# Kernel tuning notes

Hardware: AMD Instinct MI355X
Metric: run time of the kernel (lower is better)

## Reference

```python
import jax, jax.numpy as jnp
import numpy as np

GROUPS = 32
N_HEADS = 16
EPS = 1e-5


def setup_inputs() -> dict:
    key = jax.random.key(0)
    ks = jax.random.split(key, 5)
    b, c, t = 4, 1024, 1024
    return {
        "x": jax.random.normal(ks[0], (b, c, t), dtype=jnp.float32),
        "gn_weight": jnp.ones((c,), dtype=jnp.float32),
        "gn_bias": jnp.zeros((c,), dtype=jnp.float32),
        "qkv_w": jax.random.normal(ks[1], (3 * c, c), dtype=jnp.float32) * (c ** -0.5),
        "qkv_b": jax.random.normal(ks[2], (3 * c,), dtype=jnp.float32) * 0.02,
        "proj_w": jax.random.normal(ks[3], (c, c), dtype=jnp.float32) * (c ** -0.5),
        "proj_b": jax.random.normal(ks[4], (c,), dtype=jnp.float32) * 0.02,
    }


def _group_norm(x, weight, bias):
    # x: [b, c, t]; GroupNorm32 computes stats in float32 (already fp32 here)
    b, c, t = x.shape
    xg = x.reshape(b, GROUPS, c // GROUPS, t)
    mean = xg.mean(axis=(2, 3), keepdims=True)
    var = xg.var(axis=(2, 3), keepdims=True)
    xn = ((xg - mean) * jax.lax.rsqrt(var + EPS)).reshape(b, c, t)
    return xn * weight[None, :, None] + bias[None, :, None]


def reference(x, gn_weight, gn_bias, qkv_w, qkv_b, proj_w, proj_b):
    b, c, t = x.shape
    xn = _group_norm(x, gn_weight, gn_bias)
    # 1x1 Conv1d == channel matmul: [3c, c] x [b, c, t] -> [b, 3c, t]
    qkv = jnp.einsum('oc,bct->bot', qkv_w, xn) + qkv_b[None, :, None]
    ch = c // N_HEADS
    # legacy per-head interleaved layout: reshape to [b*H, 3*ch, t], split
    qkv = qkv.reshape(b * N_HEADS, 3 * ch, t)
    q, k, v = qkv[:, :ch], qkv[:, ch:2 * ch], qkv[:, 2 * ch:]
    scale = ch ** -0.25  # 1/sqrt(sqrt(ch)), applied to both q and k
    weight = jnp.einsum('bct,bcs->bts', q * scale, k * scale)  # [b*H, t, t]
    weight = jax.nn.softmax(weight.astype(jnp.float32), axis=-1).astype(weight.dtype)
    a = jnp.einsum('bts,bcs->bct', weight, v).reshape(b, c, t)
    h = jnp.einsum('oc,bct->bot', proj_w, a) + proj_b[None, :, None]
    return x + h
```

## Files before the change

### kernel.cpp

```cpp
#include <hip/hip_runtime.h>
#include <hip/hip_bf16.h>

typedef __bf16 bf16;
typedef __bf16 bf16x2 __attribute__((ext_vector_type(2)));
typedef __bf16 bf16x4 __attribute__((ext_vector_type(4)));
typedef __bf16 bf16x8 __attribute__((ext_vector_type(8)));
typedef float  f32x4  __attribute__((ext_vector_type(4)));

static __device__ __forceinline__ f32x4 mfma16(bf16x8 a, bf16x8 b, f32x4 c) {
  return __builtin_amdgcn_mfma_f32_16x16x32_bf16(a, b, c, 0, 0, 0);
}

static __device__ __forceinline__ void gload_lds16(const bf16* g, bf16* l) {
  __builtin_amdgcn_global_load_lds(
      (const __attribute__((address_space(1))) void*)g,
      (__attribute__((address_space(3))) void*)l, 16, 0, 0);
}

#define VMCNT0() asm volatile("s_waitcnt vmcnt(0)" ::: "memory")
#define BARRIER()                                        \
  do {                                                   \
    asm volatile("" ::: "memory");                       \
    __builtin_amdgcn_s_barrier();                        \
    asm volatile("" ::: "memory");                       \
  } while (0)

__global__ __launch_bounds__(256) void cvt2_kernel(const float* __restrict__ wa,
                                                   bf16* __restrict__ oa,
                                                   const float* __restrict__ wb,
                                                   bf16* __restrict__ ob) {
  int i = blockIdx.x * 256 + threadIdx.x;
  const int na4 = 3072 * 1024 / 4;
  const float* src; bf16* dst;
  if (i < na4) { src = wa; dst = oa; }
  else         { src = wb; dst = ob; i -= na4; }
  float4 v = ((const float4*)src)[i];
  bf16x4 o = { (bf16)v.x, (bf16)v.y, (bf16)v.z, (bf16)v.w };
  *(bf16x4*)(dst + 4ll * i) = o;
}

__global__ __launch_bounds__(512) void gn_kernel(const float* __restrict__ x,
                                                 const float* __restrict__ w,
                                                 const float* __restrict__ bias,
                                                 bf16* __restrict__ xnT) {
  int id = blockIdx.x;
  int b = id >> 7, g = (id >> 2) & 31, qtr = id & 3;
  const float* xb = x + ((size_t)b * 1024 + g * 32) * 1024;
  int tid = threadIdx.x;
  float s = 0.f, sq = 0.f;
  const float4* x4 = (const float4*)xb;
  for (int i = tid; i < 8192; i += 512) {
    float4 v = x4[i];
    s  += v.x + v.y + v.z + v.w;
    sq += v.x * v.x + v.y * v.y + v.z * v.z + v.w * v.w;
  }
#pragma unroll
  for (int off = 32; off; off >>= 1) { s += __shfl_down(s, off); sq += __shfl_down(sq, off); }
  __shared__ float red[16];
  int wv = tid >> 6;
  if ((tid & 63) == 0) { red[wv] = s; red[8 + wv] = sq; }
  __syncthreads();
  s = 0.f; sq = 0.f;
#pragma unroll
  for (int i = 0; i < 8; ++i) { s += red[i]; sq += red[8 + i]; }
  float mean = s * (1.f / 32768.f);
  float var  = sq * (1.f / 32768.f) - mean * mean;
  float rstd = rsqrtf(var + 1e-5f);

  __shared__ bf16 tile[64][36];
  int c = tid >> 4, q = tid & 15;
  int r = tid >> 3, q2 = tid & 7;
  float wc = w[g * 32 + c] * rstd;
  float fb = bias[g * 32 + c] - mean * wc;
  for (int t0 = qtr * 256; t0 < qtr * 256 + 256; t0 += 64) {
    float4 v = *(const float4*)(xb + (size_t)c * 1024 + t0 + q * 4);
    tile[q * 4 + 0][c] = (bf16)(v.x * wc + fb);
    tile[q * 4 + 1][c] = (bf16)(v.y * wc + fb);
    tile[q * 4 + 2][c] = (bf16)(v.z * wc + fb);
    tile[q * 4 + 3][c] = (bf16)(v.w * wc + fb);
    __syncthreads();
    *(bf16x4*)&xnT[((size_t)b * 1024 + t0 + r) * 1024 + g * 32 + q2 * 4] =
        *(bf16x4*)&tile[r][q2 * 4];
    __syncthreads();
  }
}

__global__ __launch_bounds__(512, 1) void qkv_kernel(
    const bf16* __restrict__ A, const bf16* __restrict__ Bw,
    const float* __restrict__ bias,
    bf16* __restrict__ qkT, bf16* __restrict__ vC) {
  extern __shared__ __align__(16) bf16 smem[];

  int tid = threadIdx.x, wid = tid >> 6, lane = tid & 63;
  int l15 = lane & 15, l4 = lane >> 4;
  int wr = wid >> 2, wc = wid & 3;
  int rsw = (l15 & 7) << 4;

  int sid = (blockIdx.x & 7) * 32 + (blockIdx.x >> 3);
  int bx = sid & 15, by = (sid >> 4) & 3, z = sid >> 6;
  int m0 = by * 256, n0 = bx * 192;
  const bf16* Ab = A + (size_t)z * 1024 * 1024 + (size_t)m0 * 1024;
  const bf16* Bb = Bw + (size_t)n0 * 1024;

  int srow = tid >> 3;
  int csw  = (tid & 7) ^ (srow & 7);
  auto stageA = [&](int d, int h, int kt) {
    bf16* dst = smem + d * 16384 + h * 8192;
    const bf16* src = Ab + (size_t)(h * 128) * 1024 + kt * 64 + csw * 8;
#pragma unroll
    for (int L = 0; L < 2; ++L)
      gload_lds16(src + (size_t)(L * 64 + srow) * 1024, dst + (L * 512 + wid * 64) * 8);
  };
  auto stageB = [&](int d, int kt) {
    bf16* dst = smem + 32768 + d * 12288;
    const bf16* src = Bb + kt * 64 + csw * 8;
#pragma unroll
    for (int L = 0; L < 3; ++L)
      gload_lds16(src + (size_t)(L * 64 + srow) * 1024, dst + (L * 512 + wid * 64) * 8);
  };

  f32x4 acc[8][3] = {};

  stageA(0, 0, 0); stageA(0, 1, 0); stageB(0, 0);
  VMCNT0();
  BARRIER();

  for (int t = 0; t < 16; ++t) {
    int d = t & 1;
    const char* Ab8 = (const char*)smem + d * 32768 + wr * 16384;
    const char* Bb8 = (const char*)smem + 65536 + d * 24576;

    bf16x8 bfr[3][2], af[4][2];
#pragma unroll
    for (int ni = 0; ni < 3; ++ni) {
      int rb = (wc * 48 + ni * 16 + l15) * 128;
#pragma unroll
      for (int kk = 0; kk < 2; ++kk)
        bfr[ni][kk] = *(const bf16x8*)(Bb8 + rb + ((kk * 64 + l4 * 16) ^ rsw));
    }
#pragma unroll
    for (int mi = 0; mi < 4; ++mi) {
      int rb = (mi * 16 + l15) * 128;
#pragma unroll
      for (int kk = 0; kk < 2; ++kk)
        af[mi][kk] = *(const bf16x8*)(Ab8 + rb + ((kk * 64 + l4 * 16) ^ rsw));
    }
    if (t < 15) { stageA(d ^ 1, 0, t + 1); stageA(d ^ 1, 1, t + 1); }
#pragma unroll
    for (int mi = 0; mi < 4; ++mi)
#pragma unroll
      for (int ni = 0; ni < 3; ++ni)
#pragma unroll
        for (int kk = 0; kk < 2; ++kk)
          acc[mi][ni] = mfma16(af[mi][kk], bfr[ni][kk], acc[mi][ni]);

#pragma unroll
    for (int mi = 0; mi < 4; ++mi) {
      int rb = ((4 + mi) * 16 + l15) * 128;
#pragma unroll
      for (int kk = 0; kk < 2; ++kk)
        af[mi][kk] = *(const bf16x8*)(Ab8 + rb + ((kk * 64 + l4 * 16) ^ rsw));
    }
    if (t < 15) stageB(d ^ 1, t + 1);
#pragma unroll
    for (int mi = 0; mi < 4; ++mi)
#pragma unroll
      for (int ni = 0; ni < 3; ++ni)
#pragma unroll
        for (int kk = 0; kk < 2; ++kk)
          acc[4 + mi][ni] = mfma16(af[mi][kk], bfr[ni][kk], acc[4 + mi][ni]);

    VMCNT0();
    BARRIER();
  }

  const float scale = 0.35355339059327373f;
  int h = bx;
#pragma unroll
  for (int ni = 0; ni < 3; ++ni) {
    int oin = wc * 48 + ni * 16;
    float bv = bias[n0 + oin + l15];
#pragma unroll
    for (int mi = 0; mi < 8; ++mi) {
      int tb = m0 + wr * 128 + mi * 16 + l4 * 4;
      f32x4 v = acc[mi][ni];
      if (oin < 128) {
#pragma unroll
        for (int i = 0; i < 4; ++i)
          qkT[((size_t)z * 1024 + tb + i) * 2048 + h * 128 + oin + l15] =
              (bf16)((v[i] + bv) * scale);
      } else {
        bf16x4 st = { (bf16)(v[0] + bv), (bf16)(v[1] + bv),
                      (bf16)(v[2] + bv), (bf16)(v[3] + bv) };
        *(bf16x4*)&vC[(((size_t)z * 16 + h) * 64 + (oin - 128 + l15)) * 1024 + tb] = st;
      }
    }
  }
}

template <int MODE>
__global__ __launch_bounds__(256) void gemm_kernel(
    const bf16* __restrict__ A, const bf16* __restrict__ Bw,
    const float* __restrict__ bias,
    bf16* __restrict__ qkT, bf16* __restrict__ vC,
    const float* __restrict__ xres, float* __restrict__ out) {
  __shared__ bf16 At[128 * 32];
  __shared__ bf16 Bt[128 * 32];
  int tid = threadIdx.x;
  int wid = tid >> 6, lane = tid & 63;
  int l15 = lane & 15, l4 = lane >> 4;
  int wm = wid >> 1, wn = wid & 1;
  int z = blockIdx.z;
  int m0 = blockIdx.y * 128, n0 = blockIdx.x * 128;
  const bf16* Ab = A + (size_t)z * 1024 * 1024 + (size_t)m0 * 1024;
  const bf16* Bb = Bw + (size_t)n0 * 1024;

  f32x4 acc[4][4] = {};

  for (int k0 = 0; k0 < 1024; k0 += 32) {
#pragma unroll
    for (int j = 0; j < 2; ++j) {
      int slot = j * 256 + tid;
      int row  = slot >> 2;
      int ck   = (slot & 3) ^ ((row >> 1) & 3);
      gload_lds16(Ab + (size_t)row * 1024 + k0 + ck * 8, At + (size_t)(j * 256 + wid * 64) * 8);
      gload_lds16(Bb + (size_t)row * 1024 + k0 + ck * 8, Bt + (size_t)(j * 256 + wid * 64) * 8);
    }
    __syncthreads();
    bf16x8 af[4], bfr[4];
#pragma unroll
    for (int mi = 0; mi < 4; ++mi) {
      int row = wm * 64 + mi * 16 + l15;
      int ck  = l4 ^ ((row >> 1) & 3);
      af[mi] = *(const bf16x8*)(At + row * 32 + ck * 8);
    }
#pragma unroll
    for (int nf = 0; nf < 4; ++nf) {
      int row = wn * 64 + nf * 16 + l15;
      int ck  = l4 ^ ((row >> 1) & 3);
      bfr[nf] = *(const bf16x8*)(Bt + row * 32 + ck * 8);
    }
#pragma unroll
    for (int mi = 0; mi < 4; ++mi)
#pragma unroll
      for (int nf = 0; nf < 4; ++nf)
        acc[mi][nf] = mfma16(af[mi], bfr[nf], acc[mi][nf]);
    __syncthreads();
  }

  if (MODE == 1) {
#pragma unroll
    for (int nf = 0; nf < 4; ++nf) {
      int o = n0 + wn * 64 + nf * 16 + l15;
      float bv = bias[o];
#pragma unroll
      for (int mi = 0; mi < 4; ++mi) {
        int tb = m0 + wm * 64 + mi * 16 + l4 * 4;
        size_t base = ((size_t)z * 1024 + o) * 1024 + tb;
        float4 xr = *(const float4*)(xres + base);
        f32x4 v = acc[mi][nf];
        float4 ov = { xr.x + v[0] + bv, xr.y + v[1] + bv,
                      xr.z + v[2] + bv, xr.w + v[3] + bv };
        *(float4*)(out + base) = ov;
      }
    }
  }
}

__global__ __launch_bounds__(512, 4) void attn_kernel(const bf16* __restrict__ qkT,
                                                      const bf16* __restrict__ vC,
                                                      bf16* __restrict__ aT) {
  __shared__ __align__(16) bf16 Kt[2][64 * 64];
  __shared__ __align__(16) bf16 Vt[2][64 * 64];
  __shared__ __align__(16) bf16 Pt[8][16 * 64];

  int id = blockIdx.x;
  int sid = (id & 7) * 64 + (id >> 3);
  int head = sid >> 3, tblk = sid & 7;
  int b = head >> 4, h = head & 15;
  int t0 = tblk * 128;
  int tid = threadIdx.x, wid = tid >> 6, lane = tid & 63;
  int l15 = lane & 15, l4 = lane >> 4;
  int trow = t0 + wid * 16;

  const bf16* kbase = qkT + (size_t)b * 1024 * 2048 + h * 128 + 64;
  const bf16* vbase = vC + (size_t)(b * 16 + h) * 64 * 1024;
  char* Pw = (char*)Pt[wid];
  int rsw = (l15 & 7) << 4;
  char* PwRow = Pw + l15 * 128;

  const bf16* qrow = qkT + ((size_t)b * 1024 + trow + l15) * 2048 + h * 128;
  bf16x8 qf[2];
#pragma unroll
  for (int kb = 0; kb < 2; ++kb) qf[kb] = *(const bf16x8*)(qrow + kb * 32 + l4 * 8);

  int rl = lane >> 3;
  int scol = (((lane & 7) * 16) ^ (rl << 4)) >> 1;
  int r8 = wid * 8 + rl;
  auto stage = [&](int buf, int st) {
    int s0 = st * 64;
    gload_lds16(kbase + (size_t)(s0 + r8) * 2048 + scol, &Kt[buf][wid * 512]);
    gload_lds16(vbase + (size_t)r8 * 1024 + s0 + scol, &Vt[buf][wid * 512]);
  };

  float m_run = -1e30f, l_run = 0.f;
  f32x4 oacc[4] = {};

  stage(0, 0);
  __syncthreads();

  for (int st = 0; st < 16; ++st) {
    int cur = st & 1;
    if (st < 15) stage(cur ^ 1, st + 1);

    const char* Kb = (const char*)Kt[cur];
    f32x4 sf[4];
#pragma unroll
    for (int nf = 0; nf < 4; ++nf) sf[nf] = (f32x4){0.f, 0.f, 0.f, 0.f};
    __builtin_amdgcn_s_setprio(1);
#pragma unroll
    for (int nf = 0; nf < 4; ++nf) {
      int rr = nf * 16 + l15;
#pragma unroll
      for (int kb = 0; kb < 2; ++kb) {
        bf16x8 kf = *(const bf16x8*)(Kb + rr * 128 + ((kb * 64 + l4 * 16) ^ rsw));
        sf[nf] = mfma16(kf, qf[kb], sf[nf]);
      }
    }
    __builtin_amdgcn_s_setprio(0);

    float mb;
    {
      float a0 = fmaxf(fmaxf(sf[0][0], sf[0][1]), fmaxf(sf[0][2], sf[0][3]));
      float a1 = fmaxf(fmaxf(sf[1][0], sf[1][1]), fmaxf(sf[1][2], sf[1][3]));
      float a2 = fmaxf(fmaxf(sf[2][0], sf[2][1]), fmaxf(sf[2][2], sf[2][3]));
      float a3 = fmaxf(fmaxf(sf[3][0], sf[3][1]), fmaxf(sf[3][2], sf[3][3]));
      mb = fmaxf(fmaxf(a0, a1), fmaxf(a2, a3));
    }
    mb = fmaxf(mb, __shfl_xor(mb, 16));
    mb = fmaxf(mb, __shfl_xor(mb, 32));
    if (!__all(mb - m_run <= 8.f)) {
      float mn = fmaxf(m_run, mb);
      float corr = __expf(m_run - mn);
      m_run = mn;
      l_run *= corr;
#pragma unroll
      for (int cf = 0; cf < 4; ++cf)
#pragma unroll
        for (int i = 0; i < 4; ++i) oacc[cf][i] *= corr;
    }
    float sb = 0.f;
#pragma unroll
    for (int nf = 0; nf < 4; ++nf) {
      float p0 = __expf(sf[nf][0] - m_run), p1 = __expf(sf[nf][1] - m_run);
      float p2 = __expf(sf[nf][2] - m_run), p3 = __expf(sf[nf][3] - m_run);
      sb += (p0 + p1) + (p2 + p3);
      int off = nf * 32 + l4 * 8;
      *(bf16x4*)(PwRow + (off ^ rsw)) = (bf16x4){ (bf16)p0, (bf16)p1, (bf16)p2, (bf16)p3 };
    }
    sb += __shfl_xor(sb, 16);
    sb += __shfl_xor(sb, 32);
    l_run += sb;

    const char* Vb = (const char*)Vt[cur];
    __builtin_amdgcn_s_setprio(1);
#pragma unroll
    for (int kb = 0; kb < 2; ++kb) {
      bf16x8 pf = *(const bf16x8*)(Pw + l15 * 128 + ((kb * 64 + l4 * 16) ^ rsw));
#pragma unroll
      for (int cf = 0; cf < 4; ++cf) {
        int rr = cf * 16 + l15;
        bf16x8 vf = *(const bf16x8*)(Vb + rr * 128 + ((kb * 64 + l4 * 16) ^ rsw));
        oacc[cf] = mfma16(vf, pf, oacc[cf]);
      }
    }
    __builtin_amdgcn_s_setprio(0);
    __syncthreads();
  }

  float rdiv = 1.f / l_run;
  int t = trow + l15;
#pragma unroll
  for (int cf = 0; cf < 4; ++cf) {
    bf16x4 ov = { (bf16)(oacc[cf][0] * rdiv), (bf16)(oacc[cf][1] * rdiv),
                  (bf16)(oacc[cf][2] * rdiv), (bf16)(oacc[cf][3] * rdiv) };
    *(bf16x4*)&aT[((size_t)b * 1024 + t) * 1024 + h * 64 + cf * 16 + l4 * 4] = ov;
  }
}

extern "C" void kernel_launch(void* const* d_in, const int* in_sizes, int n_in,
                              void* d_out, int out_size, void* d_ws, size_t ws_size,
                              hipStream_t stream) {
  const float* x      = (const float*)d_in[0];
  const float* gw     = (const float*)d_in[1];
  const float* gb     = (const float*)d_in[2];
  const float* qkv_w  = (const float*)d_in[3];
  const float* qkv_b  = (const float*)d_in[4];
  const float* proj_w = (const float*)d_in[5];
  const float* proj_b = (const float*)d_in[6];
  float* out = (float*)d_out;

  char* ws = (char*)d_ws;
  bf16* wq_bf = (bf16*)(ws);
  bf16* wp_bf = (bf16*)(ws + 6ll  * 1024 * 1024);
  bf16* xnT   = (bf16*)(ws + 8ll  * 1024 * 1024);
  bf16* qkT   = (bf16*)(ws + 16ll * 1024 * 1024);
  bf16* vC    = (bf16*)(ws + 32ll * 1024 * 1024);
  bf16* aT    = (bf16*)(ws + 40ll * 1024 * 1024);

  hipFuncSetAttribute(reinterpret_cast<const void*>(qkv_kernel),
                      hipFuncAttributeMaxDynamicSharedMemorySize, 114688);

  cvt2_kernel<<<dim3(4096), dim3(256), 0, stream>>>(qkv_w, wq_bf, proj_w, wp_bf);
  gn_kernel<<<dim3(512), dim3(512), 0, stream>>>(x, gw, gb, xnT);
  qkv_kernel<<<dim3(256), dim3(512), 114688, stream>>>(xnT, wq_bf, qkv_b, qkT, vC);
  attn_kernel<<<dim3(512), dim3(512), 0, stream>>>(qkT, vC, aT);
  gemm_kernel<1><<<dim3(8, 8, 4), dim3(256), 0, stream>>>(aT, wp_bf, proj_b, nullptr, nullptr, x, out);
}
```

Baseline: 108.4 us.

## Triple-buffer A tiles in QKV GEMM with partial vmcnt waits

Restructures the QKV GEMM main loop so A tiles are triple-buffered and B tiles double-buffered. Loads are issued two k-steps ahead for A, and the wait becomes vmcnt(4) instead of a full drain, so global-to-LDS loads overlap more of the MFMA work. LDS use grows from 112 KB to 144 KB per block. This is still within the 160 KB LDS per CU but leaves less headroom, and correctness depends on the vmcnt accounting matching the load issue order.

```diff
diff --git a/kernel.cpp b/kernel.cpp
--- a/kernel.cpp
+++ b/kernel.cpp
@@ -18,6 +18,7 @@
 }
 
 #define VMCNT0() asm volatile("s_waitcnt vmcnt(0)" ::: "memory")
+#define VMCNT4() asm volatile("s_waitcnt vmcnt(4)" ::: "memory")
 #define BARRIER()                                        \
   do {                                                   \
     asm volatile("" ::: "memory");                       \
@@ -104,15 +105,18 @@
 
   int srow = tid >> 3;
   int csw  = (tid & 7) ^ (srow & 7);
-  auto stageA = [&](int d, int h, int kt) {
-    bf16* dst = smem + d * 16384 + h * 8192;
-    const bf16* src = Ab + (size_t)(h * 128) * 1024 + kt * 64 + csw * 8;
-#pragma unroll
-    for (int L = 0; L < 2; ++L)
-      gload_lds16(src + (size_t)(L * 64 + srow) * 1024, dst + (L * 512 + wid * 64) * 8);
+  auto stageA = [&](int d, int kt) {
+    bf16* dst = smem + d * 16384;
+    const bf16* src = Ab + kt * 64 + csw * 8;
+#pragma unroll
+    for (int hh = 0; hh < 2; ++hh)
+#pragma unroll
+      for (int L = 0; L < 2; ++L)
+        gload_lds16(src + (size_t)(hh * 128 + L * 64 + srow) * 1024,
+                    dst + hh * 8192 + (L * 512 + wid * 64) * 8);
   };
   auto stageB = [&](int d, int kt) {
-    bf16* dst = smem + 32768 + d * 12288;
+    bf16* dst = smem + 49152 + d * 12288;
     const bf16* src = Bb + kt * 64 + csw * 8;
 #pragma unroll
     for (int L = 0; L < 3; ++L)
@@ -121,58 +125,63 @@
 
   f32x4 acc[8][3] = {};
 
-  stageA(0, 0, 0); stageA(0, 1, 0); stageB(0, 0);
+  auto compute = [&](int ta, int tb) {
+    const char* Ab8 = (const char*)smem + ta * 32768 + wr * 16384;
+    const char* Bb8 = (const char*)smem + 98304 + tb * 24576;
+    bf16x8 bfr[3][2], af[4][2];
+#pragma unroll
+    for (int ni = 0; ni < 3; ++ni) {
+      int rb = (wc * 48 + ni * 16 + l15) * 128;
+#pragma unroll
+      for (int kk = 0; kk < 2; ++kk)
+        bfr[ni][kk] = *(const bf16x8*)(Bb8 + rb + ((kk * 64 + l4 * 16) ^ rsw));
+    }
+#pragma unroll
+    for (int mi = 0; mi < 4; ++mi) {
+      int rb = (mi * 16 + l15) * 128;
+#pragma unroll
+      for (int kk = 0; kk < 2; ++kk)
+        af[mi][kk] = *(const bf16x8*)(Ab8 + rb + ((kk * 64 + l4 * 16) ^ rsw));
+    }
+#pragma unroll
+    for (int mi = 0; mi < 4; ++mi)
+#pragma unroll
+      for (int ni = 0; ni < 3; ++ni)
+#pragma unroll
+        for (int kk = 0; kk < 2; ++kk)
+          acc[mi][ni] = mfma16(af[mi][kk], bfr[ni][kk], acc[mi][ni]);
+#pragma unroll
+    for (int mi = 0; mi < 4; ++mi) {
+      int rb = ((4 + mi) * 16 + l15) * 128;
+#pragma unroll
+      for (int kk = 0; kk < 2; ++kk)
+        af[mi][kk] = *(const bf16x8*)(Ab8 + rb + ((kk * 64 + l4 * 16) ^ rsw));
+    }
+#pragma unroll
+    for (int mi = 0; mi < 4; ++mi)
+#pragma unroll
+      for (int ni = 0; ni < 3; ++ni)
+#pragma unroll
+        for (int kk = 0; kk < 2; ++kk)
+          acc[4 + mi][ni] = mfma16(af[mi][kk], bfr[ni][kk], acc[4 + mi][ni]);
+  };
+
+  stageA(0, 0); stageB(0, 0); stageA(1, 1);
+  VMCNT4();
+  BARRIER();
+
+  for (int t = 0; t < 14; ++t) {
+    stageB((t + 1) & 1, t + 1);
+    stageA((t + 2) % 3, t + 2);
+    compute(t % 3, t & 1);
+    VMCNT4();
+    BARRIER();
+  }
+  stageB(1, 15);
+  compute(2, 0);
   VMCNT0();
   BARRIER();
-
-  for (int t = 0; t < 16; ++t) {
-    int d = t & 1;
-    const char* Ab8 = (const char*)smem + d * 32768 + wr * 16384;
-    const char* Bb8 = (const char*)smem + 65536 + d * 24576;
-
-    bf16x8 bfr[3][2], af[4][2];
-#pragma unroll
-    for (int ni = 0; ni < 3; ++ni) {
-      int rb = (wc * 48 + ni * 16 + l15) * 128;
-#pragma unroll
-      for (int kk = 0; kk < 2; ++kk)
-        bfr[ni][kk] = *(const bf16x8*)(Bb8 + rb + ((kk * 64 + l4 * 16) ^ rsw));
-    }
-#pragma unroll
-    for (int mi = 0; mi < 4; ++mi) {
-      int rb = (mi * 16 + l15) * 128;
-#pragma unroll
-      for (int kk = 0; kk < 2; ++kk)
-        af[mi][kk] = *(const bf16x8*)(Ab8 + rb + ((kk * 64 + l4 * 16) ^ rsw));
-    }
-    if (t < 15) { stageA(d ^ 1, 0, t + 1); stageA(d ^ 1, 1, t + 1); }
-#pragma unroll
-    for (int mi = 0; mi < 4; ++mi)
-#pragma unroll
-      for (int ni = 0; ni < 3; ++ni)
-#pragma unroll
-        for (int kk = 0; kk < 2; ++kk)
-          acc[mi][ni] = mfma16(af[mi][kk], bfr[ni][kk], acc[mi][ni]);
-
-#pragma unroll
-    for (int mi = 0; mi < 4; ++mi) {
-      int rb = ((4 + mi) * 16 + l15) * 128;
-#pragma unroll
-      for (int kk = 0; kk < 2; ++kk)
-        af[mi][kk] = *(const bf16x8*)(Ab8 + rb + ((kk * 64 + l4 * 16) ^ rsw));
-    }
-    if (t < 15) stageB(d ^ 1, t + 1);
-#pragma unroll
-    for (int mi = 0; mi < 4; ++mi)
-#pragma unroll
-      for (int ni = 0; ni < 3; ++ni)
-#pragma unroll
-        for (int kk = 0; kk < 2; ++kk)
-          acc[4 + mi][ni] = mfma16(af[mi][kk], bfr[ni][kk], acc[4 + mi][ni]);
-
-    VMCNT0();
-    BARRIER();
-  }
+  compute(0, 1);
 
   const float scale = 0.35355339059327373f;
   int h = bx;
@@ -409,11 +418,11 @@
   bf16* aT    = (bf16*)(ws + 40ll * 1024 * 1024);
 
   hipFuncSetAttribute(reinterpret_cast<const void*>(qkv_kernel),
-                      hipFuncAttributeMaxDynamicSharedMemorySize, 114688);
+                      hipFuncAttributeMaxDynamicSharedMemorySize, 147456);
 
   cvt2_kernel<<<dim3(4096), dim3(256), 0, stream>>>(qkv_w, wq_bf, proj_w, wp_bf);
   gn_kernel<<<dim3(512), dim3(512), 0, stream>>>(x, gw, gb, xnT);
-  qkv_kernel<<<dim3(256), dim3(512), 114688, stream>>>(xnT, wq_bf, qkv_b, qkT, vC);
+  qkv_kernel<<<dim3(256), dim3(512), 147456, stream>>>(xnT, wq_bf, qkv_b, qkT, vC);
   attn_kernel<<<dim3(512), dim3(512), 0, stream>>>(qkT, vC, aT);
   gemm_kernel<1><<<dim3(8, 8, 4), dim3(256), 0, stream>>>(aT, wp_bf, proj_b, nullptr, nullptr, x, out);
 }
```

Result: no change. 107.1 us (-1.2%).
